# Optimization experiments

Measured on AMD Instinct MI355X. Metric: run time of the kernel, lower is better.

The kernel has to match this reference:

```python
import jax, jax.numpy as jnp
import numpy as np

NMS_MAX_OUTPUTS = 2000
CLS_SCORE_THRESH = 0.7
IOU_THRESH = 0.3
USE_SIDE_REFINE = False
B, N_ANCHORS, N_VALID, NUM_CLASSES = 4, 20000, 12000, 2


def setup_inputs() -> dict:
    key = jax.random.key(0)
    k = jax.random.split(key, 7)
    deltas = 0.5 * jax.random.normal(k[0], (B, N_ANCHORS, 2), jnp.float32)
    side_deltas = 0.5 * jax.random.normal(k[1], (B, N_ANCHORS, 1), jnp.float32)
    class_logits = 2.0 * jax.random.normal(k[2], (B, N_ANCHORS, NUM_CLASSES), jnp.float32)
    # CTPN-style anchors: fixed width 16, heights in [11, 280], on a ~1600px page
    cx = jax.random.uniform(k[3], (N_VALID,), jnp.float32, 8.0, 1592.0)
    cy = jax.random.uniform(k[4], (N_VALID,), jnp.float32, 0.0, 1600.0)
    h = jax.random.uniform(k[5], (N_VALID,), jnp.float32, 11.0, 280.0)
    valid_anchors = jnp.stack([cx - 8.0, cy - h * 0.5, cx + 8.0, cy + h * 0.5], axis=1)
    valid_indices = jnp.sort(
        jax.random.choice(k[6], N_ANCHORS, (N_VALID,), replace=False)
    ).astype(jnp.int32)
    return {
        "deltas": deltas,
        "side_deltas": side_deltas,
        "class_logits": class_logits,
        "valid_anchors": valid_anchors,
        "valid_indices": valid_indices,
    }


def apply_regress(deltas, side_deltas, anchors, use_side_refine):
    # deltas [B,V,2], side_deltas [B,V,1], anchors [V,4] -> [B,V,4]
    w = anchors[:, 2] - anchors[:, 0]
    h = anchors[:, 3] - anchors[:, 1]
    cx = (anchors[:, 0] + anchors[:, 2]) * 0.5
    cy = (anchors[:, 1] + anchors[:, 3]) * 0.5
    d = jnp.concatenate([deltas, side_deltas], axis=-1) * jnp.array([0.1, 0.2, 0.1], deltas.dtype)
    dy, dh, dx = d[..., 0], d[..., 1], d[..., 2]
    cy = cy + dy * h
    cx = cx + dx * w
    h = h * jnp.exp(dh)
    y1 = cy - h * 0.5
    y2 = cy + h * 0.5
    if use_side_refine:
        x1 = jnp.maximum(cx - w * 0.5, 0.0)
        x2 = cx + w * 0.5
    else:
        x1 = jnp.broadcast_to(anchors[:, 0], y1.shape)
        x2 = jnp.broadcast_to(anchors[:, 2], y1.shape)
    return jnp.stack([x1, y1, x2, y2], axis=-1)


def nms_single(boxes, scores, logits, max_out, iou_t, score_t):
    """Greedy NMS (tf.image.non_max_suppression semantics) + gather + pad_to_fixed_size."""
    V = boxes.shape[0]
    order = jnp.argsort(-jax.lax.stop_gradient(scores))
    b, s, l = boxes[order], scores[order], logits[order]
    bc = jax.lax.stop_gradient(b)  # suppression decisions are non-differentiable
    x1, y1, x2, y2 = bc[:, 0], bc[:, 1], bc[:, 2], bc[:, 3]
    areas = (x2 - x1) * (y2 - y1)
    idxs = jnp.arange(V)
    valid = jax.lax.stop_gradient(s) > score_t

    def body(i, keep):
        xx1 = jnp.maximum(x1[i], x1)
        yy1 = jnp.maximum(y1[i], y1)
        xx2 = jnp.minimum(x2[i], x2)
        yy2 = jnp.minimum(y2[i], y2)
        inter = jnp.maximum(xx2 - xx1, 0.0) * jnp.maximum(yy2 - yy1, 0.0)
        iou = inter / (areas[i] + areas - inter + 1e-10)
        sup = (iou > iou_t) & (idxs > i)
        return jnp.where(keep[i], keep & ~sup, keep)

    keep = jax.lax.fori_loop(0, V, body, valid)
    rank = jnp.cumsum(keep.astype(jnp.int32)) - 1
    sel = keep & (rank < max_out)
    dest = jnp.where(sel, rank, max_out)  # overflow rows parked at row max_out, sliced off
    tag = jnp.ones((V, 1), b.dtype)

    def pad_fixed(x):
        # append tag column of 1s for real rows, scatter to fixed size, zero-pad rest
        aug = jnp.where(sel[:, None], jnp.concatenate([x, tag], axis=1), 0.0)
        out = jnp.zeros((max_out + 1, aug.shape[1]), aug.dtype).at[dest].set(aug)
        return out[:max_out]

    return pad_fixed(b), pad_fixed(s[:, None]), pad_fixed(l)


def reference(deltas, side_deltas, class_logits, valid_anchors, valid_indices):
    d = jnp.take(deltas, valid_indices, axis=1)
    sd = jnp.take(side_deltas, valid_indices, axis=1)
    cl = jnp.take(class_logits, valid_indices, axis=1)
    class_scores = jax.nn.softmax(cl, axis=-1)
    fg_scores = jnp.max(class_scores[..., 1:], axis=-1)  # [B,V]
    proposals = apply_regress(d, sd, valid_anchors, USE_SIDE_REFINE)  # [B,V,4]
    f = lambda bb, ss, ll: nms_single(bb, ss, ll, NMS_MAX_OUTPUTS, IOU_THRESH, CLS_SCORE_THRESH)
    boxes, box_scores, out_logits = jax.vmap(f)(proposals, fg_scores, cl)
    return boxes, box_scores, out_logits
```

## Files before the change

kernel.cpp:

```cpp
#include <hip/hip_runtime.h>
#include <cstdint>
#include <cstddef>

typedef unsigned long long u64;
typedef unsigned int u32;

#define AS1 __attribute__((address_space(1)))
#define AS3 __attribute__((address_space(3)))

constexpr int kB = 4;
constexpr int kNA = 20000;
constexpr int kV = 12000;
constexpr int kCAP = 5120;
constexpr int kW = kCAP / 64;
constexpr int kIC = 256;
constexpr int kMAXOUT = 2000;
constexpr int kWGB = 80;
constexpr float kIOU = 0.3f;
constexpr float kSCORE = 0.7f;

static __device__ __forceinline__ u64 greedy64(u64 freeS, u32 d_lo, u32 d_hi) {
  u64 keptS;
  asm volatile(
      "s_mov_b64 s[40:41], %[free]\n\t"
      "s_mov_b64 s[42:43], 0\n\t"
      "GRD_%=:\n\t"
      "s_ff1_i32_b64 s44, s[40:41]\n\t"
      "s_cmp_eq_i32 s44, -1\n\t"
      "s_cbranch_scc1 GRDEND_%=\n\t"
      "s_bitset1_b64 s[42:43], s44\n\t"
      "s_bitset0_b64 s[40:41], s44\n\t"
      "v_readlane_b32 s46, %[dlo], s44\n\t"
      "v_readlane_b32 s47, %[dhi], s44\n\t"
      "s_nop 4\n\t"
      "s_andn2_b64 s[40:41], s[40:41], s[46:47]\n\t"
      "s_branch GRD_%=\n\t"
      "GRDEND_%=:\n\t"
      "s_mov_b64 %[kept], s[42:43]\n\t"
      : [kept] "=&s"(keptS)
      : [free] "s"(freeS), [dlo] "v"(d_lo), [dhi] "v"(d_hi)
      : "s40", "s41", "s42", "s43", "s44", "s45", "s46", "s47", "scc");
  return keptS;
}

__global__ __launch_bounds__(256) void stage_score(
    const float* __restrict__ deltas, const float* __restrict__ logits,
    const float* __restrict__ anchors, const int* __restrict__ vidx,
    u32* __restrict__ counts, u64* __restrict__ keys,
    float* __restrict__ rec_y1, float* __restrict__ rec_y2,
    float* __restrict__ rec_l0, float* __restrict__ rec_l1) {
  int t = blockIdx.x * 256 + threadIdx.x;
  if (t >= kB * kV) return;
  int b = t / kV, i = t - b * kV;
  int lane = threadIdx.x & 63;
  int idx = vidx[i];
  float2 lg = *(const float2*)(logits + ((size_t)b * kNA + idx) * 2);
  float score = 1.0f / (1.0f + expf(lg.x - lg.y));
  if (!(score > kSCORE)) return;
  float2 dd = *(const float2*)(deltas + ((size_t)b * kNA + idx) * 2);
  float4 a = *(const float4*)(anchors + (size_t)i * 4);
  float h = a.w - a.y;
  float cy = (a.y + a.w) * 0.5f + (dd.x * 0.1f) * h;
  float hn = h * expf(dd.y * 0.2f);
  rec_y1[t] = cy - hn * 0.5f;
  rec_y2[t] = cy + hn * 0.5f;
  rec_l0[t] = lg.x;
  rec_l1[t] = lg.y;
  u64 act = __ballot(1);
  int b0 = (int)__builtin_amdgcn_readfirstlane((u32)b);
  u64 sameb = __ballot(b == b0);
  u64 grp = (b == b0) ? sameb : (act & ~sameb);
  u32 cnt = (u32)__popcll(grp);
  int lead = (int)__ffsll((unsigned long long)grp) - 1;
  u32 base = 0;
  if (lane == lead) base = atomicAdd(&counts[b], cnt);
  base = (u32)__shfl((int)base, lead, 64);
  u32 pos = base + (u32)__popcll(grp & ((1ULL << lane) - 1ULL));
  if (pos < kCAP) {
    u64 key = ((u64)(0xFFFFFFFFu - __float_as_uint(score)) << 32) | (u32)i;
    keys[(size_t)b * kCAP + pos] = key;
  }
}

__global__ __launch_bounds__(256) void rank_sort_emit(
    const u32* __restrict__ counts, const u64* __restrict__ keys,
    const float* __restrict__ rec_y1, const float* __restrict__ rec_y2,
    const float* __restrict__ rec_l0, const float* __restrict__ rec_l1,
    const float* __restrict__ anchors,
    float4* __restrict__ sbox, float* __restrict__ sarea,
    float* __restrict__ ssc, float* __restrict__ sl0, float* __restrict__ sl1) {
  __shared__ u64 sk[kCAP];
  int b = blockIdx.x / (kCAP / 256);
  int chunk = blockIdx.x % (kCAP / 256);
  int tid = threadIdx.x;
  int cnt = (int)min(counts[b], (u32)kCAP);
  for (int e = tid; e < kCAP; e += 256)
    sk[e] = (e < cnt) ? keys[(size_t)b * kCAP + e] : ~0ULL;
  __syncthreads();
  int s = chunk * 256 + tid;
  if (s >= cnt) return;
  u64 ks = sk[s];
  int rank = 0;
  for (int j = 0; j < kCAP; j += 8) {
#pragma unroll
    for (int u = 0; u < 8; ++u) rank += (sk[j + u] < ks) ? 1 : 0;
  }
  int i = (int)(u32)ks;
  float sc = __uint_as_float(0xFFFFFFFFu - (u32)(ks >> 32));
  float x1 = anchors[(size_t)i * 4 + 0], x2 = anchors[(size_t)i * 4 + 2];
  float y1 = rec_y1[b * kV + i], y2 = rec_y2[b * kV + i];
  size_t o = (size_t)b * kCAP + rank;
  sbox[o] = make_float4(x1, y1, x2, y2);
  sarea[o] = (x2 - x1) * (y2 - y1);
  ssc[o] = sc;
  sl0[o] = rec_l0[b * kV + i];
  sl1[o] = rec_l1[b * kV + i];
}

__global__ __launch_bounds__(256) void stage_mask(
    const u32* __restrict__ counts,
    const float4* __restrict__ sbox, const float* __restrict__ sarea,
    u64* __restrict__ mask) {
  __shared__ float4 sb[4][kIC];
  __shared__ float sa[4][kIC];
  int lane = threadIdx.x & 63;
  int wv = threadIdx.x >> 6;
  int gw = blockIdx.x * 4 + wv;
  int bt = gw & 3;
  int rest = gw >> 2;
  int jb = rest % kW;
  int ic = rest / kW;
  int M = (int)min(counts[bt], (u32)kCAP);
  int W = (M + 63) >> 6;
  if (jb >= W) return;
  int ibeg = ic * kIC;
  int iend = min(min(M, jb * 64 + 64), ibeg + kIC);
  if (ibeg >= iend) return;
  const float4* pb = sbox + (size_t)bt * kCAP;
  const float* pa = sarea + (size_t)bt * kCAP;
  u64* mb = mask + (size_t)bt * ((size_t)kW * kCAP);
#pragma unroll
  for (int r = 0; r < kIC / 64; ++r) {
    int e = r * 64 + lane;
    sb[wv][e] = pb[ibeg + e];
    sa[wv][e] = pa[ibeg + e];
  }
  int j = jb * 64 + lane;
  bool jv = (j < M);
  float4 bj = make_float4(0.f, 0.f, 0.f, 0.f);
  float aj = 0.f;
  if (jv) { bj = pb[j]; aj = pa[j]; }
#pragma unroll 4
  for (int i = ibeg; i < iend; ++i) {
    float4 bi = sb[wv][i - ibeg];
    float ai = sa[wv][i - ibeg];
    float xx1 = fmaxf(bi.x, bj.x);
    float yy1 = fmaxf(bi.y, bj.y);
    float xx2 = fminf(bi.z, bj.z);
    float yy2 = fminf(bi.w, bj.w);
    float inter = fmaxf(xx2 - xx1, 0.0f) * fmaxf(yy2 - yy1, 0.0f);
    float iou = inter / (ai + aj - inter + 1e-10f);
    bool sup = jv && (j > i) && (iou > kIOU);
    u64 wm = __ballot(sup);
    if (lane == 0)
      mb[(((size_t)(i >> 6)) * kW + jb) * 64 + (i & 63)] = wm;
  }
}

__global__ __launch_bounds__(64, 1) void stage_scan(
    const u32* __restrict__ counts, const u64* __restrict__ mask,
    u64* __restrict__ pub, int* __restrict__ keepidx, u32* __restrict__ kcnt) {
  __shared__ __align__(16) u64 col[kWGB * 64];
  const int bid = blockIdx.x;
  const int bt = bid & 3;
  const int g = bid >> 2;
  const int lane = threadIdx.x;
  const int M = (int)min(counts[bt], (u32)kCAP);
  const int W = (M + 63) >> 6;
  if (g >= W) return;
  const u64* mb = mask + (size_t)bt * ((size_t)kW * kCAP);
  u64* pp = pub + (size_t)bt * (kWGB * 2);

  {
    const u64* src0 = mb + ((size_t)(lane >> 5) * kW + g) * 64 + (size_t)(lane & 31) * 2;
#pragma unroll
    for (int k = 0; k < kWGB / 2; ++k)
      __builtin_amdgcn_global_load_lds(
          (const AS1 u32*)(src0 + (size_t)(2 * k) * kW * 64),
          (AS3 u32*)&col[k * 128], 16, 0, 0);
  }
  __builtin_amdgcn_s_waitcnt(0x0070);
  const u64 diag = col[g * 64 + lane];

  u64 acc = 0;
  u32 cum = 0;
  for (int w = 0; w < g; ++w) {
    u64 colw = col[w * 64 + lane];
    u64 w0, w1;
    do {
      w0 = __hip_atomic_load(&pp[2 * w], __ATOMIC_RELAXED, __HIP_MEMORY_SCOPE_AGENT);
    } while (!(w0 >> 63));
    do {
      w1 = __hip_atomic_load(&pp[2 * w + 1], __ATOMIC_RELAXED, __HIP_MEMORY_SCOPE_AGENT);
    } while (!(w1 >> 63));
    u64 km = (u64)(u32)w0 | ((u64)(u32)w1 << 32);
    if (w == g - 1) cum = (u32)(w0 >> 32) & 0x7FFFFFFFu;
    if (km) {
      u64 v = ((km >> lane) & 1ULL) ? colw : 0ULL;
      v |= __shfl_xor((unsigned long long)v, 32, 64);
      v |= __shfl_xor((unsigned long long)v, 16, 64);
      v |= __shfl_xor((unsigned long long)v, 8, 64);
      v |= __shfl_xor((unsigned long long)v, 4, 64);
      v |= __shfl_xor((unsigned long long)v, 2, 64);
      v |= __shfl_xor((unsigned long long)v, 1, 64);
      acc |= v;
    }
  }

  const int remn = M - g * 64;
  const u64 validm = (remn >= 64) ? ~0ULL : ((1ULL << remn) - 1ULL);
  u64 keptm = 0;
  u32 cum2 = cum;
  if ((int)cum < kMAXOUT) {
    u64 freeb = ~acc & validm;
    u32 flo = __builtin_amdgcn_readfirstlane((u32)freeb);
    u32 fhi = __builtin_amdgcn_readfirstlane((u32)(freeb >> 32));
    keptm = greedy64(((u64)fhi << 32) | flo, (u32)diag, (u32)(diag >> 32));
    cum2 = cum + (u32)__popcll(keptm);
  }
  if (lane == 0) {
    u64 hi = (1ULL << 63) | ((u64)cum2 << 32);
    __hip_atomic_store(&pp[2 * g], hi | (u64)(u32)keptm,
                       __ATOMIC_RELAXED, __HIP_MEMORY_SCOPE_AGENT);
    __hip_atomic_store(&pp[2 * g + 1], hi | (u64)(u32)(keptm >> 32),
                       __ATOMIC_RELAXED, __HIP_MEMORY_SCOPE_AGENT);
  }
  if ((keptm >> lane) & 1ULL) {
    int rank = (int)cum + (int)__popcll(keptm & ((1ULL << lane) - 1ULL));
    if (rank < kMAXOUT) keepidx[bt * kMAXOUT + rank] = g * 64 + lane;
  }
  if (g == W - 1 && lane == 0) kcnt[bt] = min(cum2, (u32)kMAXOUT);
}

__global__ __launch_bounds__(256) void stage_out(
    const u32* __restrict__ kcnt, const int* __restrict__ keepidx,
    const float4* __restrict__ sbox, const float* __restrict__ ssc,
    const float* __restrict__ sl0, const float* __restrict__ sl1,
    float* __restrict__ out) {
  int t = blockIdx.x * 256 + threadIdx.x;
  if (t >= kB * kMAXOUT) return;
  int b = t / kMAXOUT, r = t - b * kMAXOUT;
  if (r >= (int)kcnt[b]) return;
  int i = keepidx[t];
  size_t o = (size_t)b * kCAP + i;
  float4 bx = sbox[o];
  float* boxes = out;
  float* bscores = out + (size_t)kB * kMAXOUT * 5;
  float* blogits = out + (size_t)kB * kMAXOUT * 7;
  boxes[(size_t)t * 5 + 0] = bx.x;
  boxes[(size_t)t * 5 + 1] = bx.y;
  boxes[(size_t)t * 5 + 2] = bx.z;
  boxes[(size_t)t * 5 + 3] = bx.w;
  boxes[(size_t)t * 5 + 4] = 1.0f;
  bscores[(size_t)t * 2 + 0] = ssc[o];
  bscores[(size_t)t * 2 + 1] = 1.0f;
  blogits[(size_t)t * 3 + 0] = sl0[o];
  blogits[(size_t)t * 3 + 1] = sl1[o];
  blogits[(size_t)t * 3 + 2] = 1.0f;
}

extern "C" void kernel_launch(void* const* d_in, const int* in_sizes, int n_in,
                              void* d_out, int out_size, void* d_ws, size_t ws_size,
                              hipStream_t stream) {
  const float* deltas = (const float*)d_in[0];
  const float* logits = (const float*)d_in[2];
  const float* anchors = (const float*)d_in[3];
  const int* vidx = (const int*)d_in[4];
  float* out = (float*)d_out;

  char* p = (char*)d_ws;
  auto take = [&](size_t bytes) -> char* {
    char* r = p;
    p += (bytes + 255) & ~(size_t)255;
    return r;
  };
  u32* counts = (u32*)take(kB * sizeof(u32));
  u32* kcnt = (u32*)take(kB * sizeof(u32));
  u64* pub = (u64*)take((size_t)kB * kWGB * 2 * sizeof(u64));
  u64* keys = (u64*)take((size_t)kB * kCAP * sizeof(u64));
  float* rec_y1 = (float*)take((size_t)kB * kV * sizeof(float));
  float* rec_y2 = (float*)take((size_t)kB * kV * sizeof(float));
  float* rec_l0 = (float*)take((size_t)kB * kV * sizeof(float));
  float* rec_l1 = (float*)take((size_t)kB * kV * sizeof(float));
  float4* sbox = (float4*)take((size_t)kB * kCAP * sizeof(float4));
  float* sarea = (float*)take((size_t)kB * kCAP * sizeof(float));
  float* ssc = (float*)take((size_t)kB * kCAP * sizeof(float));
  float* sl0 = (float*)take((size_t)kB * kCAP * sizeof(float));
  float* sl1 = (float*)take((size_t)kB * kCAP * sizeof(float));
  int* keepidx = (int*)take((size_t)kB * kMAXOUT * sizeof(int));
  u64* mask = (u64*)take((size_t)kB * kCAP * kW * sizeof(u64) + 4096);

  (void)hipMemsetAsync(out, 0, (size_t)out_size * sizeof(float), stream);
  (void)hipMemsetAsync(counts, 0, 5632, stream);

  stage_score<<<(kB * kV + 255) / 256, 256, 0, stream>>>(
      deltas, logits, anchors, vidx, counts, keys, rec_y1, rec_y2, rec_l0, rec_l1);
  rank_sort_emit<<<kB * (kCAP / 256), 256, 0, stream>>>(
      counts, keys, rec_y1, rec_y2, rec_l0, rec_l1, anchors,
      sbox, sarea, ssc, sl0, sl1);
  stage_mask<<<kB * kW * (kCAP / kIC) / 4, 256, 0, stream>>>(
      counts, sbox, sarea, mask);
  stage_scan<<<kB * kWGB, 64, 0, stream>>>(counts, mask, pub, keepidx, kcnt);
  stage_out<<<(kB * kMAXOUT + 255) / 256, 256, 0, stream>>>(
      kcnt, keepidx, sbox, ssc, sl0, sl1, out);
}
```

Baseline: 368.8 us.

## Process two 64-row blocks per scan workgroup to halve the serial publish chain

The NMS scan kernel now gives each workgroup two consecutive 64-candidate blocks instead of one. That halves the number of workgroups in the serial dependency chain and the cross-workgroup flag polls. Each group loads a 128-wide column slice into LDS and resolves both blocks locally, feeding the first block's kept set into the second before publishing four flag words. The cumulative count is now recomputed from popcounts instead of being published. In exchange, each group does twice the LDS loading and wave-OR reductions per predecessor, and there are fewer groups to run in parallel.

New measurement: 365.9 us. Within noise of the previous version (-0.8%).

```diff
diff --git a/kernel.cpp b/kernel.cpp
--- a/kernel.cpp
+++ b/kernel.cpp
@@ -15,7 +15,7 @@
 constexpr int kW = kCAP / 64;
 constexpr int kIC = 256;
 constexpr int kMAXOUT = 2000;
-constexpr int kWGB = 80;
+constexpr int kGPB = 40;
 constexpr float kIOU = 0.3f;
 constexpr float kSCORE = 0.7f;
 
@@ -41,6 +41,16 @@
       : [free] "s"(freeS), [dlo] "v"(d_lo), [dhi] "v"(d_hi)
       : "s40", "s41", "s42", "s43", "s44", "s45", "s46", "s47", "scc");
   return keptS;
+}
+
+__device__ __forceinline__ u64 waveOr64(u64 v) {
+  v |= __shfl_xor((unsigned long long)v, 32, 64);
+  v |= __shfl_xor((unsigned long long)v, 16, 64);
+  v |= __shfl_xor((unsigned long long)v, 8, 64);
+  v |= __shfl_xor((unsigned long long)v, 4, 64);
+  v |= __shfl_xor((unsigned long long)v, 2, 64);
+  v |= __shfl_xor((unsigned long long)v, 1, 64);
+  return v;
 }
 
 __global__ __launch_bounds__(256) void stage_score(
@@ -170,76 +180,99 @@
 __global__ __launch_bounds__(64, 1) void stage_scan(
     const u32* __restrict__ counts, const u64* __restrict__ mask,
     u64* __restrict__ pub, int* __restrict__ keepidx, u32* __restrict__ kcnt) {
-  __shared__ __align__(16) u64 col[kWGB * 64];
+  __shared__ __align__(16) u64 col[80 * 128];
   const int bid = blockIdx.x;
   const int bt = bid & 3;
   const int g = bid >> 2;
   const int lane = threadIdx.x;
   const int M = (int)min(counts[bt], (u32)kCAP);
   const int W = (M + 63) >> 6;
-  if (g >= W) return;
+  const int blk0 = 2 * g, blk1 = 2 * g + 1;
+  if (blk0 >= W) return;
   const u64* mb = mask + (size_t)bt * ((size_t)kW * kCAP);
-  u64* pp = pub + (size_t)bt * (kWGB * 2);
-
-  {
-    const u64* src0 = mb + ((size_t)(lane >> 5) * kW + g) * 64 + (size_t)(lane & 31) * 2;
+  u64* pp = pub + (size_t)(bt * kGPB) * 4;
+
 #pragma unroll
-    for (int k = 0; k < kWGB / 2; ++k)
-      __builtin_amdgcn_global_load_lds(
-          (const AS1 u32*)(src0 + (size_t)(2 * k) * kW * 64),
-          (AS3 u32*)&col[k * 128], 16, 0, 0);
-  }
+  for (int b = 0; b < 80; ++b)
+    __builtin_amdgcn_global_load_lds(
+        (const AS1 u32*)(mb + ((size_t)b * kW + blk0) * 64 + (size_t)lane * 2),
+        (AS3 u32*)&col[b * 128], 16, 0, 0);
   __builtin_amdgcn_s_waitcnt(0x0070);
-  const u64 diag = col[g * 64 + lane];
-
-  u64 acc = 0;
+
+  u64 acc0 = 0, acc1 = 0;
   u32 cum = 0;
   for (int w = 0; w < g; ++w) {
-    u64 colw = col[w * 64 + lane];
-    u64 w0, w1;
+    const u64* q = pp + (size_t)w * 4;
+    u64 a0, a1, a2, a3;
     do {
-      w0 = __hip_atomic_load(&pp[2 * w], __ATOMIC_RELAXED, __HIP_MEMORY_SCOPE_AGENT);
-    } while (!(w0 >> 63));
-    do {
-      w1 = __hip_atomic_load(&pp[2 * w + 1], __ATOMIC_RELAXED, __HIP_MEMORY_SCOPE_AGENT);
-    } while (!(w1 >> 63));
-    u64 km = (u64)(u32)w0 | ((u64)(u32)w1 << 32);
-    if (w == g - 1) cum = (u32)(w0 >> 32) & 0x7FFFFFFFu;
-    if (km) {
-      u64 v = ((km >> lane) & 1ULL) ? colw : 0ULL;
-      v |= __shfl_xor((unsigned long long)v, 32, 64);
-      v |= __shfl_xor((unsigned long long)v, 16, 64);
-      v |= __shfl_xor((unsigned long long)v, 8, 64);
-      v |= __shfl_xor((unsigned long long)v, 4, 64);
-      v |= __shfl_xor((unsigned long long)v, 2, 64);
-      v |= __shfl_xor((unsigned long long)v, 1, 64);
-      acc |= v;
+      a0 = __hip_atomic_load(q + 0, __ATOMIC_RELAXED, __HIP_MEMORY_SCOPE_AGENT);
+      a1 = __hip_atomic_load(q + 1, __ATOMIC_RELAXED, __HIP_MEMORY_SCOPE_AGENT);
+      a2 = __hip_atomic_load(q + 2, __ATOMIC_RELAXED, __HIP_MEMORY_SCOPE_AGENT);
+      a3 = __hip_atomic_load(q + 3, __ATOMIC_RELAXED, __HIP_MEMORY_SCOPE_AGENT);
+    } while (((a0 & a1 & a2 & a3) >> 63) == 0);
+    u64 km0 = (u64)(u32)a0 | ((u64)(u32)a1 << 32);
+    u64 km1 = (u64)(u32)a2 | ((u64)(u32)a3 << 32);
+    cum += (u32)__popcll(km0) + (u32)__popcll(km1);
+    if (km0 | km1) {
+      bool k0 = (km0 >> lane) & 1ULL, k1 = (km1 >> lane) & 1ULL;
+      u64 v = (k0 ? col[(2 * w) * 128 + lane] : 0ULL) |
+              (k1 ? col[(2 * w + 1) * 128 + lane] : 0ULL);
+      u64 u = (k0 ? col[(2 * w) * 128 + 64 + lane] : 0ULL) |
+              (k1 ? col[(2 * w + 1) * 128 + 64 + lane] : 0ULL);
+      acc0 |= waveOr64(v);
+      acc1 |= waveOr64(u);
     }
   }
 
-  const int remn = M - g * 64;
-  const u64 validm = (remn >= 64) ? ~0ULL : ((1ULL << remn) - 1ULL);
-  u64 keptm = 0;
-  u32 cum2 = cum;
-  if ((int)cum < kMAXOUT) {
-    u64 freeb = ~acc & validm;
+  u64 keptm0 = 0;
+  const u32 cum0 = cum;
+  if ((int)cum0 < kMAXOUT) {
+    int remn = M - blk0 * 64;
+    u64 validm = (remn >= 64) ? ~0ULL : ((1ULL << remn) - 1ULL);
+    u64 freeb = ~acc0 & validm;
     u32 flo = __builtin_amdgcn_readfirstlane((u32)freeb);
     u32 fhi = __builtin_amdgcn_readfirstlane((u32)(freeb >> 32));
-    keptm = greedy64(((u64)fhi << 32) | flo, (u32)diag, (u32)(diag >> 32));
-    cum2 = cum + (u32)__popcll(keptm);
-  }
+    u64 diag = col[blk0 * 128 + lane];
+    keptm0 = greedy64(((u64)fhi << 32) | flo, (u32)diag, (u32)(diag >> 32));
+  }
+  cum = cum0 + (u32)__popcll(keptm0);
+  if (keptm0) {
+    u64 x = ((keptm0 >> lane) & 1ULL) ? col[blk0 * 128 + 64 + lane] : 0ULL;
+    acc1 |= waveOr64(x);
+  }
+  u64 keptm1 = 0;
+  const u32 cum1 = cum;
+  if (blk1 < W && (int)cum1 < kMAXOUT) {
+    int remn = M - blk1 * 64;
+    u64 validm = (remn >= 64) ? ~0ULL : ((1ULL << remn) - 1ULL);
+    u64 freeb = ~acc1 & validm;
+    u32 flo = __builtin_amdgcn_readfirstlane((u32)freeb);
+    u32 fhi = __builtin_amdgcn_readfirstlane((u32)(freeb >> 32));
+    u64 diag = col[blk1 * 128 + 64 + lane];
+    keptm1 = greedy64(((u64)fhi << 32) | flo, (u32)diag, (u32)(diag >> 32));
+  }
+  cum = cum1 + (u32)__popcll(keptm1);
+
   if (lane == 0) {
-    u64 hi = (1ULL << 63) | ((u64)cum2 << 32);
-    __hip_atomic_store(&pp[2 * g], hi | (u64)(u32)keptm,
+    const u64 F = 1ULL << 63;
+    __hip_atomic_store(&pp[(size_t)g * 4 + 0], F | (u64)(u32)keptm0,
                        __ATOMIC_RELAXED, __HIP_MEMORY_SCOPE_AGENT);
-    __hip_atomic_store(&pp[2 * g + 1], hi | (u64)(u32)(keptm >> 32),
+    __hip_atomic_store(&pp[(size_t)g * 4 + 1], F | (u64)(u32)(keptm0 >> 32),
                        __ATOMIC_RELAXED, __HIP_MEMORY_SCOPE_AGENT);
-  }
-  if ((keptm >> lane) & 1ULL) {
-    int rank = (int)cum + (int)__popcll(keptm & ((1ULL << lane) - 1ULL));
-    if (rank < kMAXOUT) keepidx[bt * kMAXOUT + rank] = g * 64 + lane;
-  }
-  if (g == W - 1 && lane == 0) kcnt[bt] = min(cum2, (u32)kMAXOUT);
+    __hip_atomic_store(&pp[(size_t)g * 4 + 2], F | (u64)(u32)keptm1,
+                       __ATOMIC_RELAXED, __HIP_MEMORY_SCOPE_AGENT);
+    __hip_atomic_store(&pp[(size_t)g * 4 + 3], F | (u64)(u32)(keptm1 >> 32),
+                       __ATOMIC_RELAXED, __HIP_MEMORY_SCOPE_AGENT);
+  }
+  if ((keptm0 >> lane) & 1ULL) {
+    int rank = (int)cum0 + (int)__popcll(keptm0 & ((1ULL << lane) - 1ULL));
+    if (rank < kMAXOUT) keepidx[bt * kMAXOUT + rank] = blk0 * 64 + lane;
+  }
+  if ((keptm1 >> lane) & 1ULL) {
+    int rank = (int)cum1 + (int)__popcll(keptm1 & ((1ULL << lane) - 1ULL));
+    if (rank < kMAXOUT) keepidx[bt * kMAXOUT + rank] = blk1 * 64 + lane;
+  }
+  if (lane == 0 && g == (W - 1) / 2) kcnt[bt] = min(cum, (u32)kMAXOUT);
 }
 
 __global__ __launch_bounds__(256) void stage_out(
@@ -286,7 +319,7 @@
   };
   u32* counts = (u32*)take(kB * sizeof(u32));
   u32* kcnt = (u32*)take(kB * sizeof(u32));
-  u64* pub = (u64*)take((size_t)kB * kWGB * 2 * sizeof(u64));
+  u64* pub = (u64*)take((size_t)kB * kGPB * 4 * sizeof(u64));
   u64* keys = (u64*)take((size_t)kB * kCAP * sizeof(u64));
   float* rec_y1 = (float*)take((size_t)kB * kV * sizeof(float));
   float* rec_y2 = (float*)take((size_t)kB * kV * sizeof(float));
@@ -310,7 +343,7 @@
       sbox, sarea, ssc, sl0, sl1);
   stage_mask<<<kB * kW * (kCAP / kIC) / 4, 256, 0, stream>>>(
       counts, sbox, sarea, mask);
-  stage_scan<<<kB * kWGB, 64, 0, stream>>>(counts, mask, pub, keepidx, kcnt);
+  stage_scan<<<kB * kGPB, 64, 0, stream>>>(counts, mask, pub, keepidx, kcnt);
   stage_out<<<(kB * kMAXOUT + 255) / 256, 256, 0, stream>>>(
       kcnt, keepidx, sbox, ssc, sl0, sl1, out);
 }
```
